# Performance work log

Hardware: AMD Instinct MI355X
Metric: run time of the kernel (lower is better)

Reference implementation:

```python
import jax, jax.numpy as jnp
import numpy as np

N, C, H, W = 16, 128, 128, 128


def setup_inputs() -> dict:
    key = jax.random.key(0)
    ks = jax.random.split(key, 7)
    s = 0.02
    return {
        "x": jax.random.normal(ks[0], (N, C, H, W), dtype=jnp.float32),
        "w_key": jax.random.normal(ks[1], (C, C), dtype=jnp.float32) * s,
        "b_key": jax.random.normal(ks[2], (C,), dtype=jnp.float32) * s,
        "w_query": jax.random.normal(ks[3], (C, C), dtype=jnp.float32) * s,
        "b_query": jax.random.normal(ks[4], (C,), dtype=jnp.float32) * s,
        "w_value": jax.random.normal(ks[5], (C, C), dtype=jnp.float32) * s,
        "b_value": jax.random.normal(ks[6], (C,), dtype=jnp.float32) * s,
        "gamma": jnp.zeros((1,), dtype=jnp.float32),
    }


def _conv1x1(x, w, b):
    # 1x1 conv: (N,C,H,W) x (O,C) -> (N,O,H,W)
    return jnp.einsum('nchw,oc->nohw', x, w) + b[None, :, None, None]


def reference(x, w_key, b_key, w_query, b_query, w_value, b_value, gamma):
    k = _conv1x1(x, w_key, b_key)
    q = _conv1x1(x, w_query, b_query)
    v = _conv1x1(x, w_value, b_value)
    k_size = x.shape[1]  # output_channel
    scale = jnp.asarray(k_size, x.dtype) ** 0.5
    # similarity[n,o,w,v] = sum_h k[n,o,h,w] * q[n,o,h,v]  (k^T over H @ q)
    sim = jnp.einsum('nohw,nohv->nowv', k, q) / scale
    # softmax over dim=2 (the first W axis)
    attn = jax.nn.softmax(sim, axis=2)
    # out[n,o,h,v] = sum_w v[n,o,h,w] * attn[n,o,w,v]
    out = jnp.einsum('nohw,nowv->nohv', v, attn)
    return gamma[0] * out + x
```

## Files before the change

kernel.cpp:

```cpp
#include <hip/hip_runtime.h>
#include <hip/hip_bf16.h>
#include <math.h>

#define CN      128
#define HWN     16384
#define NBATCH  16
#define PLANE   (CN * HWN)
#define TSTRIDE ((size_t)NBATCH * PLANE)

typedef __attribute__((ext_vector_type(8))) short  short8;
typedef __attribute__((ext_vector_type(4))) float  float4v;

__device__ __forceinline__ unsigned short f2b(float f) {
    __hip_bfloat16 h = __float2bfloat16(f);
    return *reinterpret_cast<unsigned short*>(&h);
}
__device__ __forceinline__ unsigned packbf(float lo, float hi) {
    return (unsigned)f2b(lo) | ((unsigned)f2b(hi) << 16);
}

__global__ void prep_kernel(const float* __restrict__ wk, const float* __restrict__ bk,
                            const float* __restrict__ wq, const float* __restrict__ bq,
                            const float* __restrict__ wv, const float* __restrict__ bv,
                            unsigned short* __restrict__ wbf, float* __restrict__ bias)
{
    int i = blockIdx.x * 256 + threadIdx.x;
    int tensor = i >> 14, oc = i & 16383;
    const float* w = tensor == 0 ? wk : (tensor == 1 ? wq : wv);
    wbf[i] = f2b(w[oc]);
    if (i < 384) {
        const float* b = i < 128 ? bk : (i < 256 ? bq : bv);
        bias[i] = b[i & 127];
    }
}

__global__ __launch_bounds__(256) void kqv_kernel(
    const float* __restrict__ x, const unsigned short* __restrict__ wbf,
    const float* __restrict__ bias, unsigned short* __restrict__ kqv)
{
    __shared__ unsigned Xl[64 * 68];

    const int n   = blockIdx.y;
    const int hw0 = blockIdx.x * 64;
    const int t    = threadIdx.x;
    const int lane = t & 63, wv = t >> 6;
    const int l15  = lane & 15, quad = lane >> 4;

    {
        const int hwg = (t & 15) * 4;
        const int c0  = (t >> 4) * 8;
        const float* xp = x + (size_t)n * PLANE + (size_t)c0 * HWN + hw0 + hwg;
        float v[8][4];
        #pragma unroll
        for (int j = 0; j < 8; ++j)
            *(float4*)v[j] = *(const float4*)(xp + (size_t)j * HWN);
        #pragma unroll
        for (int jj = 0; jj < 4; ++jj) {
            uint4 u;
            u.x = packbf(v[0][jj], v[1][jj]);
            u.y = packbf(v[2][jj], v[3][jj]);
            u.z = packbf(v[4][jj], v[5][jj]);
            u.w = packbf(v[6][jj], v[7][jj]);
            *(uint4*)&Xl[(hwg + jj) * 68 + c0 / 2] = u;
        }
    }
    __syncthreads();

    short8 afr[4][4];
    #pragma unroll
    for (int mt = 0; mt < 4; ++mt)
        #pragma unroll
        for (int k = 0; k < 4; ++k)
            afr[mt][k] = *(const short8*)&Xl[(mt * 16 + l15) * 68 + quad * 4 + k * 16];

    #pragma unroll
    for (int nt = 0; nt < 6; ++nt) {
        const int ob = wv * 96 + nt * 16;
        const int tensor = ob >> 7;
        const int oc = (ob & 127) + l15;
        short8 wfr[4];
        #pragma unroll
        for (int k = 0; k < 4; ++k)
            wfr[k] = *(const short8*)&wbf[(ob + l15) * CN + quad * 8 + k * 32];
        const float b = bias[ob + l15];
        unsigned short* dst = kqv + (size_t)tensor * TSTRIDE
                            + ((size_t)n * CN + oc) * HWN + hw0 + quad * 4;
        #pragma unroll
        for (int mt = 0; mt < 4; ++mt) {
            float4v acc = {b, b, b, b};
            #pragma unroll
            for (int k = 0; k < 4; ++k)
                acc = __builtin_amdgcn_mfma_f32_16x16x32_bf16(afr[mt][k], wfr[k], acc, 0, 0, 0);
            uint2 u;
            u.x = packbf(acc[0], acc[1]);
            u.y = packbf(acc[2], acc[3]);
            *(uint2*)(dst + mt * 16) = u;
        }
    }
}

__global__ __launch_bounds__(256) void attn_kernel(
    const unsigned short* __restrict__ kqv, const float* __restrict__ x,
    const float* __restrict__ gamma, float* __restrict__ out)
{
    __shared__ unsigned lds[17408];
    unsigned* Kt = lds;
    unsigned* Qt = lds + 8704;
    unsigned short* At = (unsigned short*)lds;

    const int no = blockIdx.x;
    const unsigned short* Kg = kqv + (size_t)no * HWN;
    const unsigned short* Qg = Kg + TSTRIDE;
    const unsigned short* Vg = Kg + 2 * TSTRIDE;

    const int t = threadIdx.x, lane = t & 63, wv = t >> 6;
    const int l15 = lane & 15, quad = lane >> 4;

    #pragma unroll
    for (int p = 0; p < 8; ++p) {
        const int w  = (p & 1) * 64 + lane;
        const int h0 = ((p >> 1) * 4 + wv) * 8;
        unsigned short kv[8], qv[8];
        #pragma unroll
        for (int j = 0; j < 8; ++j) {
            kv[j] = Kg[(h0 + j) * 128 + w];
            qv[j] = Qg[(h0 + j) * 128 + w];
        }
        uint4 a, b;
        a.x = (unsigned)kv[0] | ((unsigned)kv[1] << 16); a.y = (unsigned)kv[2] | ((unsigned)kv[3] << 16);
        a.z = (unsigned)kv[4] | ((unsigned)kv[5] << 16); a.w = (unsigned)kv[6] | ((unsigned)kv[7] << 16);
        b.x = (unsigned)qv[0] | ((unsigned)qv[1] << 16); b.y = (unsigned)qv[2] | ((unsigned)qv[3] << 16);
        b.z = (unsigned)qv[4] | ((unsigned)qv[5] << 16); b.w = (unsigned)qv[6] | ((unsigned)qv[7] << 16);
        *(uint4*)&Kt[w * 68 + h0 / 2] = a;
        *(uint4*)&Qt[w * 68 + h0 / 2] = b;
    }
    __syncthreads();

    const int v0 = wv * 32;
    float4v acc1[2][8];
    #pragma unroll
    for (int mt = 0; mt < 2; ++mt)
        #pragma unroll
        for (int nt = 0; nt < 8; ++nt) acc1[mt][nt] = (float4v){0.f, 0.f, 0.f, 0.f};

    {
        short8 afr[2][4];
        #pragma unroll
        for (int mt = 0; mt < 2; ++mt)
            #pragma unroll
            for (int k = 0; k < 4; ++k)
                afr[mt][k] = *(const short8*)&Qt[(v0 + mt * 16 + l15) * 68 + quad * 4 + k * 16];
        #pragma unroll
        for (int nt = 0; nt < 8; ++nt) {
            short8 bfr[4];
            #pragma unroll
            for (int k = 0; k < 4; ++k)
                bfr[k] = *(const short8*)&Kt[(nt * 16 + l15) * 68 + quad * 4 + k * 16];
            #pragma unroll
            for (int mt = 0; mt < 2; ++mt)
                #pragma unroll
                for (int k = 0; k < 4; ++k)
                    acc1[mt][nt] = __builtin_amdgcn_mfma_f32_16x16x32_bf16(afr[mt][k], bfr[k], acc1[mt][nt], 0, 0, 0);
        }
    }
    __syncthreads();

    const float sc = 0.08838834764831845f;
    #pragma unroll
    for (int mt = 0; mt < 2; ++mt)
        #pragma unroll
        for (int r = 0; r < 4; ++r) {
            float m = -INFINITY;
            #pragma unroll
            for (int nt = 0; nt < 8; ++nt) {
                acc1[mt][nt][r] *= sc;
                m = fmaxf(m, acc1[mt][nt][r]);
            }
            #pragma unroll
            for (int d = 1; d < 16; d <<= 1) m = fmaxf(m, __shfl_xor(m, d, 64));
            float s = 0.f;
            #pragma unroll
            for (int nt = 0; nt < 8; ++nt) {
                const float e = __expf(acc1[mt][nt][r] - m);
                acc1[mt][nt][r] = e;
                s += e;
            }
            #pragma unroll
            for (int d = 1; d < 16; d <<= 1) s += __shfl_xor(s, d, 64);
            const float inv = 1.0f / s;
            const int v = v0 + mt * 16 + quad * 4 + r;
            #pragma unroll
            for (int nt = 0; nt < 8; ++nt)
                At[v * 136 + nt * 16 + l15] = f2b(acc1[mt][nt][r] * inv);
        }

    float4v acc2[2][8];
    #pragma unroll
    for (int mt = 0; mt < 2; ++mt)
        #pragma unroll
        for (int nt = 0; nt < 8; ++nt) acc2[mt][nt] = (float4v){0.f, 0.f, 0.f, 0.f};

    {
        short8 pfr[2][4];
        #pragma unroll
        for (int mt = 0; mt < 2; ++mt)
            #pragma unroll
            for (int k = 0; k < 4; ++k)
                pfr[mt][k] = *(const short8*)&At[(v0 + mt * 16 + l15) * 136 + quad * 8 + k * 32];
        #pragma unroll
        for (int nt = 0; nt < 8; ++nt) {
            short8 vfr[4];
            #pragma unroll
            for (int k = 0; k < 4; ++k)
                vfr[k] = *(const short8*)&Vg[(nt * 16 + l15) * 128 + quad * 8 + k * 32];
            #pragma unroll
            for (int mt = 0; mt < 2; ++mt)
                #pragma unroll
                for (int k = 0; k < 4; ++k)
                    acc2[mt][nt] = __builtin_amdgcn_mfma_f32_16x16x32_bf16(pfr[mt][k], vfr[k], acc2[mt][nt], 0, 0, 0);
        }
    }

    const float g = gamma[0];
    const float* xp = x + (size_t)no * HWN;
    float*       op = out + (size_t)no * HWN;
    #pragma unroll
    for (int mt = 0; mt < 2; ++mt)
        #pragma unroll
        for (int nt = 0; nt < 8; ++nt) {
            const int h    = nt * 16 + l15;
            const int vcol = v0 + mt * 16 + quad * 4;
            const int idx  = h * 128 + vcol;
            float4 xv = *(const float4*)(xp + idx);
            float4 ov;
            ov.x = fmaf(g, acc2[mt][nt][0], xv.x);
            ov.y = fmaf(g, acc2[mt][nt][1], xv.y);
            ov.z = fmaf(g, acc2[mt][nt][2], xv.z);
            ov.w = fmaf(g, acc2[mt][nt][3], xv.w);
            *(float4*)(op + idx) = ov;
        }
}

extern "C" void kernel_launch(void* const* d_in, const int* in_sizes, int n_in,
                              void* d_out, int out_size, void* d_ws, size_t ws_size,
                              hipStream_t stream) {
    const float* x     = (const float*)d_in[0];
    const float* wk    = (const float*)d_in[1];
    const float* bk    = (const float*)d_in[2];
    const float* wq    = (const float*)d_in[3];
    const float* bq    = (const float*)d_in[4];
    const float* wv    = (const float*)d_in[5];
    const float* bv    = (const float*)d_in[6];
    const float* gamma = (const float*)d_in[7];
    float* out = (float*)d_out;

    unsigned short* wbf  = (unsigned short*)d_ws;
    float*          bias = (float*)((char*)d_ws + (192 << 10));
    unsigned short* kqv  = (unsigned short*)((char*)d_ws + (256 << 10));

    prep_kernel<<<192, 256, 0, stream>>>(wk, bk, wq, bq, wv, bv, wbf, bias);
    dim3 gA(HWN / 64, NBATCH);
    kqv_kernel<<<gA, 256, 0, stream>>>(x, wbf, bias, kqv);
    attn_kernel<<<NBATCH * CN, 256, 0, stream>>>(kqv, x, gamma, out);
}
```

Before: 443.5 us.

## Store K and Q transposed from projection kernel to skip transpose in attention

```diff
diff --git a/kernel.cpp b/kernel.cpp
--- a/kernel.cpp
+++ b/kernel.cpp
@@ -34,7 +34,84 @@
     }
 }
 
-__global__ __launch_bounds__(256) void kqv_kernel(
+__global__ __launch_bounds__(256) void kq_kernel(
+    const float* __restrict__ x, const unsigned short* __restrict__ wbf,
+    const float* __restrict__ bias, unsigned short* __restrict__ kqv)
+{
+    __shared__ unsigned Xl[128 * 68];
+
+    const int bx = blockIdx.x;
+    const int n  = blockIdx.y;
+    const int s8 = bx & 7, m4 = (bx >> 3) & 3, ht = bx >> 5;
+    const int w0 = (s8 * 4 + m4) * 4;
+    const int h0 = ht * 32;
+
+    const int t = threadIdx.x, lane = t & 63, wv = t >> 6;
+    const int l15 = lane & 15, quad = lane >> 4;
+
+    {
+        const int c0  = (t & 15) * 8;
+        const int hl2 = (t >> 4) * 2;
+        const float* xp = x + (size_t)n * PLANE + (size_t)c0 * HWN
+                        + (h0 + hl2) * 128 + w0;
+        float vv[2][8][4];
+        #pragma unroll
+        for (int j = 0; j < 8; ++j)
+            #pragma unroll
+            for (int p = 0; p < 2; ++p)
+                *(float4*)vv[p][j] = *(const float4*)(xp + (size_t)j * HWN + p * 128);
+        #pragma unroll
+        for (int p = 0; p < 2; ++p)
+            #pragma unroll
+            for (int wl = 0; wl < 4; ++wl) {
+                uint4 u;
+                u.x = packbf(vv[p][0][wl], vv[p][1][wl]);
+                u.y = packbf(vv[p][2][wl], vv[p][3][wl]);
+                u.z = packbf(vv[p][4][wl], vv[p][5][wl]);
+                u.w = packbf(vv[p][6][wl], vv[p][7][wl]);
+                *(uint4*)&Xl[(wl * 32 + hl2 + p) * 68 + c0 / 2] = u;
+            }
+    }
+    __syncthreads();
+
+    const int ob = wv * 64;
+    short8 wfr[4][4];
+    #pragma unroll
+    for (int nt = 0; nt < 4; ++nt)
+        #pragma unroll
+        for (int k = 0; k < 4; ++k)
+            wfr[nt][k] = *(const short8*)&wbf[(ob + nt * 16 + l15) * CN + quad * 8 + k * 32];
+    float bs[4];
+    #pragma unroll
+    for (int nt = 0; nt < 4; ++nt) bs[nt] = bias[ob + nt * 16 + l15];
+
+    const int tensor = wv >> 1;
+    const int obase  = (wv & 1) * 64;
+
+    #pragma unroll
+    for (int mt = 0; mt < 8; ++mt) {
+        short8 afr[4];
+        #pragma unroll
+        for (int k = 0; k < 4; ++k)
+            afr[k] = *(const short8*)&Xl[(mt * 16 + l15) * 68 + quad * 4 + k * 16];
+        const int wl = mt >> 1;
+        const int hh = h0 + (mt & 1) * 16 + quad * 4;
+        #pragma unroll
+        for (int nt = 0; nt < 4; ++nt) {
+            float4v acc = {bs[nt], bs[nt], bs[nt], bs[nt]};
+            #pragma unroll
+            for (int k = 0; k < 4; ++k)
+                acc = __builtin_amdgcn_mfma_f32_16x16x32_bf16(afr[k], wfr[nt][k], acc, 0, 0, 0);
+            const int o = obase + nt * 16 + l15;
+            unsigned short* dst = kqv + (size_t)tensor * TSTRIDE
+                                + ((size_t)n * CN + o) * HWN + (w0 + wl) * 128 + hh;
+            uint2 u; u.x = packbf(acc[0], acc[1]); u.y = packbf(acc[2], acc[3]);
+            *(uint2*)dst = u;
+        }
+    }
+}
+
+__global__ __launch_bounds__(256) void v_kernel(
     const float* __restrict__ x, const unsigned short* __restrict__ wbf,
     const float* __restrict__ bias, unsigned short* __restrict__ kqv)
 {
@@ -42,9 +119,8 @@
 
     const int n   = blockIdx.y;
     const int hw0 = blockIdx.x * 64;
-    const int t    = threadIdx.x;
-    const int lane = t & 63, wv = t >> 6;
-    const int l15  = lane & 15, quad = lane >> 4;
+    const int t = threadIdx.x, lane = t & 63, wv = t >> 6;
+    const int l15 = lane & 15, quad = lane >> 4;
 
     {
         const int hwg = (t & 15) * 4;
@@ -57,10 +133,8 @@
         #pragma unroll
         for (int jj = 0; jj < 4; ++jj) {
             uint4 u;
-            u.x = packbf(v[0][jj], v[1][jj]);
-            u.y = packbf(v[2][jj], v[3][jj]);
-            u.z = packbf(v[4][jj], v[5][jj]);
-            u.w = packbf(v[6][jj], v[7][jj]);
+            u.x = packbf(v[0][jj], v[1][jj]); u.y = packbf(v[2][jj], v[3][jj]);
+            u.z = packbf(v[4][jj], v[5][jj]); u.w = packbf(v[6][jj], v[7][jj]);
             *(uint4*)&Xl[(hwg + jj) * 68 + c0 / 2] = u;
         }
     }
@@ -74,26 +148,23 @@
             afr[mt][k] = *(const short8*)&Xl[(mt * 16 + l15) * 68 + quad * 4 + k * 16];
 
     #pragma unroll
-    for (int nt = 0; nt < 6; ++nt) {
-        const int ob = wv * 96 + nt * 16;
-        const int tensor = ob >> 7;
-        const int oc = (ob & 127) + l15;
+    for (int nt = 0; nt < 2; ++nt) {
+        const int ob = 256 + wv * 32 + nt * 16;
         short8 wfr[4];
         #pragma unroll
         for (int k = 0; k < 4; ++k)
             wfr[k] = *(const short8*)&wbf[(ob + l15) * CN + quad * 8 + k * 32];
         const float b = bias[ob + l15];
-        unsigned short* dst = kqv + (size_t)tensor * TSTRIDE
-                            + ((size_t)n * CN + oc) * HWN + hw0 + quad * 4;
+        const int oc = wv * 32 + nt * 16 + l15;
+        unsigned short* dst = kqv + 2 * TSTRIDE + ((size_t)n * CN + oc) * HWN
+                            + hw0 + quad * 4;
         #pragma unroll
         for (int mt = 0; mt < 4; ++mt) {
             float4v acc = {b, b, b, b};
             #pragma unroll
             for (int k = 0; k < 4; ++k)
                 acc = __builtin_amdgcn_mfma_f32_16x16x32_bf16(afr[mt][k], wfr[k], acc, 0, 0, 0);
-            uint2 u;
-            u.x = packbf(acc[0], acc[1]);
-            u.y = packbf(acc[2], acc[3]);
+            uint2 u; u.x = packbf(acc[0], acc[1]); u.y = packbf(acc[2], acc[3]);
             *(uint2*)(dst + mt * 16) = u;
         }
     }
@@ -103,10 +174,7 @@
     const unsigned short* __restrict__ kqv, const float* __restrict__ x,
     const float* __restrict__ gamma, float* __restrict__ out)
 {
-    __shared__ unsigned lds[17408];
-    unsigned* Kt = lds;
-    unsigned* Qt = lds + 8704;
-    unsigned short* At = (unsigned short*)lds;
+    __shared__ unsigned short At[128 * 136];
 
     const int no = blockIdx.x;
     const unsigned short* Kg = kqv + (size_t)no * HWN;
@@ -115,28 +183,8 @@
 
     const int t = threadIdx.x, lane = t & 63, wv = t >> 6;
     const int l15 = lane & 15, quad = lane >> 4;
-
-    #pragma unroll
-    for (int p = 0; p < 8; ++p) {
-        const int w  = (p & 1) * 64 + lane;
-        const int h0 = ((p >> 1) * 4 + wv) * 8;
-        unsigned short kv[8], qv[8];
-        #pragma unroll
-        for (int j = 0; j < 8; ++j) {
-            kv[j] = Kg[(h0 + j) * 128 + w];
-            qv[j] = Qg[(h0 + j) * 128 + w];
-        }
-        uint4 a, b;
-        a.x = (unsigned)kv[0] | ((unsigned)kv[1] << 16); a.y = (unsigned)kv[2] | ((unsigned)kv[3] << 16);
-        a.z = (unsigned)kv[4] | ((unsigned)kv[5] << 16); a.w = (unsigned)kv[6] | ((unsigned)kv[7] << 16);
-        b.x = (unsigned)qv[0] | ((unsigned)qv[1] << 16); b.y = (unsigned)qv[2] | ((unsigned)qv[3] << 16);
-        b.z = (unsigned)qv[4] | ((unsigned)qv[5] << 16); b.w = (unsigned)qv[6] | ((unsigned)qv[7] << 16);
-        *(uint4*)&Kt[w * 68 + h0 / 2] = a;
-        *(uint4*)&Qt[w * 68 + h0 / 2] = b;
-    }
-    __syncthreads();
-
     const int v0 = wv * 32;
+
     float4v acc1[2][8];
     #pragma unroll
     for (int mt = 0; mt < 2; ++mt)
@@ -149,13 +197,13 @@
         for (int mt = 0; mt < 2; ++mt)
             #pragma unroll
             for (int k = 0; k < 4; ++k)
-                afr[mt][k] = *(const short8*)&Qt[(v0 + mt * 16 + l15) * 68 + quad * 4 + k * 16];
+                afr[mt][k] = *(const short8*)&Qg[(v0 + mt * 16 + l15) * 128 + quad * 8 + k * 32];
         #pragma unroll
         for (int nt = 0; nt < 8; ++nt) {
             short8 bfr[4];
             #pragma unroll
             for (int k = 0; k < 4; ++k)
-                bfr[k] = *(const short8*)&Kt[(nt * 16 + l15) * 68 + quad * 4 + k * 16];
+                bfr[k] = *(const short8*)&Kg[(nt * 16 + l15) * 128 + quad * 8 + k * 32];
             #pragma unroll
             for (int mt = 0; mt < 2; ++mt)
                 #pragma unroll
@@ -163,7 +211,6 @@
                     acc1[mt][nt] = __builtin_amdgcn_mfma_f32_16x16x32_bf16(afr[mt][k], bfr[k], acc1[mt][nt], 0, 0, 0);
         }
     }
-    __syncthreads();
 
     const float sc = 0.08838834764831845f;
     #pragma unroll
@@ -259,7 +306,9 @@
     unsigned short* kqv  = (unsigned short*)((char*)d_ws + (256 << 10));
 
     prep_kernel<<<192, 256, 0, stream>>>(wk, bk, wq, bq, wv, bv, wbf, bias);
-    dim3 gA(HWN / 64, NBATCH);
-    kqv_kernel<<<gA, 256, 0, stream>>>(x, wbf, bias, kqv);
+    dim3 gK(128, NBATCH);
+    kq_kernel<<<gK, 256, 0, stream>>>(x, wbf, bias, kqv);
+    dim3 gV(HWN / 64, NBATCH);
+    v_kernel<<<gV, 256, 0, stream>>>(x, wbf, bias, kqv);
     attn_kernel<<<NBATCH * CN, 256, 0, stream>>>(kqv, x, gamma, out);
 }
```

Result: slower. 490.9 us (+10.7%).

## Write K and Q transposed from conv kernel so attention reads MFMA fragments directly

Applied to the files above, without the earlier changes.

```diff
diff --git a/kernel.cpp b/kernel.cpp
--- a/kernel.cpp
+++ b/kernel.cpp
@@ -34,79 +34,111 @@
     }
 }
 
-__global__ __launch_bounds__(256) void kqv_kernel(
+__device__ __forceinline__ int swzkey(int s) { return ((s ^ (s >> 4)) & 7) << 2; }
+
+template<bool TRANS>
+__device__ __forceinline__ void conv_phase(
+    const unsigned* Xl, const unsigned short* __restrict__ wbf,
+    const float* __restrict__ bias, unsigned short* kqv_t,
+    int tens, int h0, int w0, int wv, int l15, int quad)
+{
+    #pragma unroll
+    for (int og = 0; og < 2; ++og) {
+        float bs[4];
+        #pragma unroll
+        for (int ni = 0; ni < 4; ++ni)
+            bs[ni] = bias[tens * 128 + og * 64 + ni * 16 + l15];
+
+        float4v acc[4][4];
+        #pragma unroll
+        for (int mi = 0; mi < 4; ++mi)
+            #pragma unroll
+            for (int ni = 0; ni < 4; ++ni)
+                acc[mi][ni] = (float4v){bs[ni], bs[ni], bs[ni], bs[ni]};
+
+        #pragma unroll
+        for (int k = 0; k < 4; ++k) {
+            short8 afr[4];
+            #pragma unroll
+            for (int mi = 0; mi < 4; ++mi) {
+                const int mt = wv * 4 + mi;
+                const int s  = TRANS ? (l15 * 16 + mt) : (mt * 16 + l15);
+                afr[mi] = *(const short8*)&Xl[s * 64 + ((k * 16 + quad * 4) ^ swzkey(s))];
+            }
+            #pragma unroll
+            for (int ni = 0; ni < 4; ++ni) {
+                const short8 wfr = *(const short8*)
+                    &wbf[(size_t)(tens * 128 + og * 64 + ni * 16 + l15) * CN + quad * 8 + k * 32];
+                #pragma unroll
+                for (int mi = 0; mi < 4; ++mi)
+                    acc[mi][ni] = __builtin_amdgcn_mfma_f32_16x16x32_bf16(afr[mi], wfr, acc[mi][ni], 0, 0, 0);
+            }
+        }
+
+        #pragma unroll
+        for (int ni = 0; ni < 4; ++ni) {
+            const int o = og * 64 + ni * 16 + l15;
+            unsigned short* dst0 = kqv_t + (size_t)o * HWN;
+            #pragma unroll
+            for (int mi = 0; mi < 4; ++mi) {
+                const int mt  = wv * 4 + mi;
+                const int idx = TRANS ? ((w0 + mt) * 128 + h0 + quad * 4)
+                                      : ((h0 + mt) * 128 + w0 + quad * 4);
+                uint2 u;
+                u.x = packbf(acc[mi][ni][0], acc[mi][ni][1]);
+                u.y = packbf(acc[mi][ni][2], acc[mi][ni][3]);
+                *(uint2*)(dst0 + idx) = u;
+            }
+        }
+    }
+}
+
+__global__ __launch_bounds__(256) void conv_kernel(
     const float* __restrict__ x, const unsigned short* __restrict__ wbf,
     const float* __restrict__ bias, unsigned short* __restrict__ kqv)
 {
-    __shared__ unsigned Xl[64 * 68];
+    __shared__ unsigned Xl[256 * 64];
 
     const int n   = blockIdx.y;
-    const int hw0 = blockIdx.x * 64;
-    const int t    = threadIdx.x;
-    const int lane = t & 63, wv = t >> 6;
-    const int l15  = lane & 15, quad = lane >> 4;
+    const int tid = blockIdx.x;
+    const int h0  = (tid >> 3) * 16, w0 = (tid & 7) * 16;
+
+    const int th = threadIdx.x, lane = th & 63, wv = th >> 6;
+    const int l15 = lane & 15, quad = lane >> 4;
 
     {
-        const int hwg = (t & 15) * 4;
-        const int c0  = (t >> 4) * 8;
-        const float* xp = x + (size_t)n * PLANE + (size_t)c0 * HWN + hw0 + hwg;
-        float v[8][4];
-        #pragma unroll
-        for (int j = 0; j < 8; ++j)
-            *(float4*)v[j] = *(const float4*)(xp + (size_t)j * HWN);
-        #pragma unroll
-        for (int jj = 0; jj < 4; ++jj) {
-            uint4 u;
-            u.x = packbf(v[0][jj], v[1][jj]);
-            u.y = packbf(v[2][jj], v[3][jj]);
-            u.z = packbf(v[4][jj], v[5][jj]);
-            u.w = packbf(v[6][jj], v[7][jj]);
-            *(uint4*)&Xl[(hwg + jj) * 68 + c0 / 2] = u;
+        const int sh = lane & 15, swq = lane >> 4;
+        const float* xp = x + (size_t)n * PLANE + (h0 + sh) * 128 + w0 + swq * 4;
+        #pragma unroll
+        for (int b = 0; b < 4; ++b) {
+            const int cb = wv * 32 + b * 8;
+            float v[8][4];
+            #pragma unroll
+            for (int j = 0; j < 8; ++j)
+                *(float4*)v[j] = *(const float4*)(xp + (size_t)(cb + j) * HWN);
+            #pragma unroll
+            for (int wi = 0; wi < 4; ++wi) {
+                const int s = sh * 16 + swq * 4 + wi;
+                uint4 u;
+                u.x = packbf(v[0][wi], v[1][wi]); u.y = packbf(v[2][wi], v[3][wi]);
+                u.z = packbf(v[4][wi], v[5][wi]); u.w = packbf(v[6][wi], v[7][wi]);
+                *(uint4*)&Xl[s * 64 + ((wv * 16 + b * 4) ^ swzkey(s))] = u;
+            }
         }
     }
     __syncthreads();
 
-    short8 afr[4][4];
-    #pragma unroll
-    for (int mt = 0; mt < 4; ++mt)
-        #pragma unroll
-        for (int k = 0; k < 4; ++k)
-            afr[mt][k] = *(const short8*)&Xl[(mt * 16 + l15) * 68 + quad * 4 + k * 16];
-
-    #pragma unroll
-    for (int nt = 0; nt < 6; ++nt) {
-        const int ob = wv * 96 + nt * 16;
-        const int tensor = ob >> 7;
-        const int oc = (ob & 127) + l15;
-        short8 wfr[4];
-        #pragma unroll
-        for (int k = 0; k < 4; ++k)
-            wfr[k] = *(const short8*)&wbf[(ob + l15) * CN + quad * 8 + k * 32];
-        const float b = bias[ob + l15];
-        unsigned short* dst = kqv + (size_t)tensor * TSTRIDE
-                            + ((size_t)n * CN + oc) * HWN + hw0 + quad * 4;
-        #pragma unroll
-        for (int mt = 0; mt < 4; ++mt) {
-            float4v acc = {b, b, b, b};
-            #pragma unroll
-            for (int k = 0; k < 4; ++k)
-                acc = __builtin_amdgcn_mfma_f32_16x16x32_bf16(afr[mt][k], wfr[k], acc, 0, 0, 0);
-            uint2 u;
-            u.x = packbf(acc[0], acc[1]);
-            u.y = packbf(acc[2], acc[3]);
-            *(uint2*)(dst + mt * 16) = u;
-        }
-    }
+    unsigned short* base = kqv + ((size_t)n * CN) * HWN;
+    conv_phase<true >(Xl, wbf, bias, base,               0, h0, w0, wv, l15, quad);
+    conv_phase<true >(Xl, wbf, bias, base + TSTRIDE,     1, h0, w0, wv, l15, quad);
+    conv_phase<false>(Xl, wbf, bias, base + 2 * TSTRIDE, 2, h0, w0, wv, l15, quad);
 }
 
 __global__ __launch_bounds__(256) void attn_kernel(
     const unsigned short* __restrict__ kqv, const float* __restrict__ x,
     const float* __restrict__ gamma, float* __restrict__ out)
 {
-    __shared__ unsigned lds[17408];
-    unsigned* Kt = lds;
-    unsigned* Qt = lds + 8704;
-    unsigned short* At = (unsigned short*)lds;
+    __shared__ unsigned short At[128 * 136];
 
     const int no = blockIdx.x;
     const unsigned short* Kg = kqv + (size_t)no * HWN;
@@ -115,28 +147,8 @@
 
     const int t = threadIdx.x, lane = t & 63, wv = t >> 6;
     const int l15 = lane & 15, quad = lane >> 4;
-
-    #pragma unroll
-    for (int p = 0; p < 8; ++p) {
-        const int w  = (p & 1) * 64 + lane;
-        const int h0 = ((p >> 1) * 4 + wv) * 8;
-        unsigned short kv[8], qv[8];
-        #pragma unroll
-        for (int j = 0; j < 8; ++j) {
-            kv[j] = Kg[(h0 + j) * 128 + w];
-            qv[j] = Qg[(h0 + j) * 128 + w];
-        }
-        uint4 a, b;
-        a.x = (unsigned)kv[0] | ((unsigned)kv[1] << 16); a.y = (unsigned)kv[2] | ((unsigned)kv[3] << 16);
-        a.z = (unsigned)kv[4] | ((unsigned)kv[5] << 16); a.w = (unsigned)kv[6] | ((unsigned)kv[7] << 16);
-        b.x = (unsigned)qv[0] | ((unsigned)qv[1] << 16); b.y = (unsigned)qv[2] | ((unsigned)qv[3] << 16);
-        b.z = (unsigned)qv[4] | ((unsigned)qv[5] << 16); b.w = (unsigned)qv[6] | ((unsigned)qv[7] << 16);
-        *(uint4*)&Kt[w * 68 + h0 / 2] = a;
-        *(uint4*)&Qt[w * 68 + h0 / 2] = b;
-    }
-    __syncthreads();
-
     const int v0 = wv * 32;
+
     float4v acc1[2][8];
     #pragma unroll
     for (int mt = 0; mt < 2; ++mt)
@@ -149,13 +161,13 @@
         for (int mt = 0; mt < 2; ++mt)
             #pragma unroll
             for (int k = 0; k < 4; ++k)
-                afr[mt][k] = *(const short8*)&Qt[(v0 + mt * 16 + l15) * 68 + quad * 4 + k * 16];
+                afr[mt][k] = *(const short8*)&Qg[(v0 + mt * 16 + l15) * 128 + quad * 8 + k * 32];
         #pragma unroll
         for (int nt = 0; nt < 8; ++nt) {
             short8 bfr[4];
             #pragma unroll
             for (int k = 0; k < 4; ++k)
-                bfr[k] = *(const short8*)&Kt[(nt * 16 + l15) * 68 + quad * 4 + k * 16];
+                bfr[k] = *(const short8*)&Kg[(nt * 16 + l15) * 128 + quad * 8 + k * 32];
             #pragma unroll
             for (int mt = 0; mt < 2; ++mt)
                 #pragma unroll
@@ -163,7 +175,6 @@
                     acc1[mt][nt] = __builtin_amdgcn_mfma_f32_16x16x32_bf16(afr[mt][k], bfr[k], acc1[mt][nt], 0, 0, 0);
         }
     }
-    __syncthreads();
 
     const float sc = 0.08838834764831845f;
     #pragma unroll
@@ -259,7 +270,7 @@
     unsigned short* kqv  = (unsigned short*)((char*)d_ws + (256 << 10));
 
     prep_kernel<<<192, 256, 0, stream>>>(wk, bk, wq, bq, wv, bv, wbf, bias);
-    dim3 gA(HWN / 64, NBATCH);
-    kqv_kernel<<<gA, 256, 0, stream>>>(x, wbf, bias, kqv);
+    dim3 gC(64, NBATCH);
+    conv_kernel<<<gC, 256, 0, stream>>>(x, wbf, bias, kqv);
     attn_kernel<<<NBATCH * CN, 256, 0, stream>>>(kqv, x, gamma, out);
 }
```

Measured after the change: 473.6 us. 6.8% more time.
